# Performance work log

Measured on AMD Instinct MI355X. Metric: run time of the kernel, lower is better.

The kernel has to match this reference:

```python
import jax, jax.numpy as jnp
import numpy as np

DIM = 768
NUM_HEADS = 12
N_TOKENS = 4096


def setup_inputs() -> dict:
    key = jax.random.key(0)
    k_x, k_qkv, k_proj, k_pb = jax.random.split(key, 4)
    x = jax.random.normal(k_x, (N_TOKENS, DIM), dtype=jnp.float32)
    # nn.Linear(dim, dim*3, bias=False): weight shape (3*dim, dim)
    w_qkv = jax.random.normal(k_qkv, (3 * DIM, DIM), dtype=jnp.float32) * (DIM ** -0.5)
    # nn.Linear(dim, dim): weight (dim, dim), bias (dim,)
    w_proj = jax.random.normal(k_proj, (DIM, DIM), dtype=jnp.float32) * (DIM ** -0.5)
    b_proj = jax.random.normal(k_pb, (DIM,), dtype=jnp.float32) * 0.01
    return {"x": x, "w_qkv": w_qkv, "w_proj": w_proj, "b_proj": b_proj}


def reference(x, w_qkv, w_proj, b_proj):
    N, C = x.shape
    H = NUM_HEADS
    hd = C // H
    scale = hd ** -0.5
    qkv = (x @ w_qkv.T).reshape(N, 3, H, hd)  # (N, 3, H, hd)
    q = qkv[:, 0]  # (N, H, hd)
    k = qkv[:, 1]
    v = qkv[:, 2]
    # full NxN score matrix per head, as in the original (non-flash) code
    attn = jnp.einsum("nhd,mhd->hnm", q, k) * scale  # (H, N, N)
    attn = jax.nn.softmax(attn, axis=-1)
    out = jnp.einsum("hnm,mhd->nhd", attn, v).reshape(N, C)  # (N, C)
    return out @ w_proj.T + b_proj
```

## Files before the change

kernel.cpp:

```cpp
#include <hip/hip_runtime.h>
#include <hip/hip_bf16.h>

typedef __bf16 bf16_t;
typedef __attribute__((ext_vector_type(8))) __bf16 bf16x8;
typedef __attribute__((ext_vector_type(4))) __bf16 bf16x4;
typedef __attribute__((ext_vector_type(4))) short s16x4;
typedef __attribute__((ext_vector_type(4))) float f32x4;
typedef __attribute__((ext_vector_type(4))) _Float16 f16x4;

#define NTOK 4096
#define DIM  768
#define NH   12
#define HD   64
#define NSPLIT 4
#define KHALF (NTOK / NSPLIT)
#define XSZ  (NTOK * DIM)
#define WQSZ (3 * DIM * DIM)
#define WPSZ (DIM * DIM)
#define SCALE_L2E 0.18033688011112042f
#define SOFTMAX_C 12.0f

__device__ __forceinline__ bf16x8 load8(const bf16_t* p) {
    return *reinterpret_cast<const bf16x8*>(p);
}
__device__ __forceinline__ void store8(bf16_t* p, bf16x8 v) {
    *reinterpret_cast<bf16x8*>(p) = v;
}
__device__ __forceinline__ void gl2lds16(const bf16_t* g, bf16_t* l) {
    __builtin_amdgcn_global_load_lds(
        (const __attribute__((address_space(1))) void*)g,
        (__attribute__((address_space(3))) void*)l, 16, 0, 0);
}

__global__ __launch_bounds__(256) void cvt_kernel(
    const float* __restrict__ x, const float* __restrict__ wq,
    const float* __restrict__ wp,
    bf16_t* __restrict__ xb, bf16_t* __restrict__ wqb, bf16_t* __restrict__ wpb)
{
    size_t i = ((size_t)blockIdx.x * 256 + threadIdx.x) * 4;
    const float* src; bf16_t* dst; size_t off;
    if (i < XSZ)             { src = x;  dst = xb;  off = i; }
    else if (i < XSZ + WQSZ) { src = wq; dst = wqb; off = i - XSZ; }
    else                     { src = wp; dst = wpb; off = i - XSZ - WQSZ; }
    float4 v = *reinterpret_cast<const float4*>(src + off);
    bf16x4 o = { (bf16_t)v.x, (bf16_t)v.y, (bf16_t)v.z, (bf16_t)v.w };
    *reinterpret_cast<bf16x4*>(dst + off) = o;
}

__global__ __launch_bounds__(256) void qkv_gemm_kernel(
    const bf16_t* __restrict__ X, const bf16_t* __restrict__ W,
    bf16_t* __restrict__ Qo, bf16_t* __restrict__ Ko, bf16_t* __restrict__ Vt)
{
    __shared__ __align__(16) bf16_t As[128 * 32];
    __shared__ __align__(16) bf16_t Bs[128 * 32];
    const int tid  = threadIdx.x;
    const int wave = tid >> 6, lane = tid & 63;
    const int lr = lane & 15, lq = lane >> 4;
    const int M0 = blockIdx.x * 128;
    const int N0 = blockIdx.y * 128;
    const int wm = (wave >> 1) * 64, wn = (wave & 1) * 64;

    const int g_row = wave * 32 + (lane >> 2);
    const int g_col = (lane & 3) * 8;

    f32x4 acc[4][4] = {};

    for (int k0 = 0; k0 < DIM; k0 += 32) {
        #pragma unroll
        for (int c = 0; c < 2; ++c) {
            gl2lds16(&X[(size_t)(M0 + g_row + c * 16) * DIM + k0 + g_col],
                     &As[(wave * 32 + c * 16) * 32]);
            gl2lds16(&W[(size_t)(N0 + g_row + c * 16) * DIM + k0 + g_col],
                     &Bs[(wave * 32 + c * 16) * 32]);
        }
        __syncthreads();
        bf16x8 af[4], bfr[4];
        #pragma unroll
        for (int i = 0; i < 4; ++i) af[i]  = load8(&As[(wm + i * 16 + lr) * 32 + lq * 8]);
        #pragma unroll
        for (int i = 0; i < 4; ++i) bfr[i] = load8(&Bs[(wn + i * 16 + lr) * 32 + lq * 8]);
        #pragma unroll
        for (int r = 0; r < 4; ++r)
            #pragma unroll
            for (int c = 0; c < 4; ++c)
                acc[r][c] = __builtin_amdgcn_mfma_f32_16x16x32_bf16(af[r], bfr[c], acc[r][c], 0, 0, 0);
        __syncthreads();
    }

    const int t = N0 / DIM;
    if (t == 2) {
        #pragma unroll
        for (int r = 0; r < 4; ++r)
            #pragma unroll
            for (int c = 0; c < 4; ++c) {
                int m0 = M0 + wm + r * 16 + lq * 4;
                int rem = N0 + wn + c * 16 + lr - 2 * DIM;
                int hh = rem >> 6, d = rem & 63;
                bf16x4 v = { (bf16_t)acc[r][c][0], (bf16_t)acc[r][c][1],
                             (bf16_t)acc[r][c][2], (bf16_t)acc[r][c][3] };
                *reinterpret_cast<bf16x4*>(&Vt[((size_t)hh * HD + d) * NTOK + m0]) = v;
            }
    } else {
        #pragma unroll
        for (int r = 0; r < 4; ++r)
            #pragma unroll
            for (int c = 0; c < 4; ++c)
                #pragma unroll
                for (int reg = 0; reg < 4; ++reg) {
                    int m = M0 + wm + r * 16 + lq * 4 + reg;
                    int rem = N0 + wn + c * 16 + lr - t * DIM;
                    int hh = rem >> 6, d = rem & 63;
                    float v = acc[r][c][reg];
                    if (t == 0) Qo[(hh * NTOK + m) * HD + d] = (bf16_t)(v * SCALE_L2E);
                    else        Ko[(hh * NTOK + m) * HD + d] = (bf16_t)v;
                }
    }
}

__global__ __launch_bounds__(256) void flash_attn_kernel(
    const bf16_t* __restrict__ Qb, const bf16_t* __restrict__ Kb,
    const bf16_t* __restrict__ Vtb, _Float16* __restrict__ Opart,
    float* __restrict__ Lpart)
{
    __shared__ __align__(16) bf16_t Ks[2][64 * 64];
    __shared__ __align__(16) bf16_t Vs[2][64 * 64];
    const int tid  = threadIdx.x;
    const int wave = tid >> 6, lane = tid & 63;
    const int lr = lane & 15, lq = lane >> 4;
    const int h  = blockIdx.y;
    const int q0 = blockIdx.x * 128;
    const int sp = blockIdx.z;
    const int kt0 = sp * KHALF;
    const int NIT = KHALF / 64;

    const int sw_st = ((tid & 7) ^ ((tid >> 3) & 7)) * 8;
    const int kc0   = (lq ^ (lr & 7)) * 8;
    const int kc1   = ((4 + lq) ^ (lr & 7)) * 8;
    int vc[4];
    #pragma unroll
    for (int g = 0; g < 4; ++g)
        vc[g] = ((2 * g + (lq >> 1)) ^ (lr & 7)) * 8 + (lq & 1) * 4;

    const bf16_t* qrowA = &Qb[((size_t)h * NTOK + q0 + wave * 32 + lr) * HD];
    const bf16_t* qrowB = qrowA + 16 * HD;
    bf16x8 qa0 = load8(&qrowA[lq * 8]);
    bf16x8 qa1 = load8(&qrowA[32 + lq * 8]);
    bf16x8 qb0 = load8(&qrowB[lq * 8]);
    bf16x8 qb1 = load8(&qrowB[32 + lq * 8]);

    float la = 0.f, lb = 0.f;
    f32x4 oA[4] = {}, oB[4] = {};
    const f32x4 mc = { -SOFTMAX_C, -SOFTMAX_C, -SOFTMAX_C, -SOFTMAX_C };

    const int srA = tid >> 3;
    const int scA = (tid & 7) * 8;
    const bf16_t* kbase = &Kb[(size_t)h * NTOK * HD];
    const bf16_t* vbase = &Vtb[(size_t)h * HD * NTOK];

    bf16x8 pk0 = load8(&kbase[(size_t)(kt0 + srA) * HD + scA]);
    bf16x8 pk1 = load8(&kbase[(size_t)(kt0 + srA + 32) * HD + scA]);
    bf16x8 pv0 = load8(&vbase[(size_t)srA * NTOK + kt0 + scA]);
    bf16x8 pv1 = load8(&vbase[(size_t)(srA + 32) * NTOK + kt0 + scA]);

    for (int it = 0; it < NIT; ++it) {
        const int kt  = kt0 + it * 64;
        const int buf = it & 1;
        store8(&Ks[buf][srA * 64 + sw_st],        pk0);
        store8(&Ks[buf][(srA + 32) * 64 + sw_st], pk1);
        store8(&Vs[buf][srA * 64 + sw_st],        pv0);
        store8(&Vs[buf][(srA + 32) * 64 + sw_st], pv1);
        __syncthreads();

        if (it + 1 < NIT) {
            const int kn = kt + 64;
            pk0 = load8(&kbase[(size_t)(kn + srA) * HD + scA]);
            pk1 = load8(&kbase[(size_t)(kn + srA + 32) * HD + scA]);
            pv0 = load8(&vbase[(size_t)srA * NTOK + kn + scA]);
            pv1 = load8(&vbase[(size_t)(srA + 32) * NTOK + kn + scA]);
        }

        f32x4 sa[4], sb[4];
        __builtin_amdgcn_s_setprio(1);
        #pragma unroll
        for (int g = 0; g < 4; ++g) {
            bf16x8 k0 = load8(&Ks[buf][(g * 16 + lr) * 64 + kc0]);
            bf16x8 k1 = load8(&Ks[buf][(g * 16 + lr) * 64 + kc1]);
            f32x4 za = mc, zb = mc;
            za = __builtin_amdgcn_mfma_f32_16x16x32_bf16(k0, qa0, za, 0, 0, 0);
            za = __builtin_amdgcn_mfma_f32_16x16x32_bf16(k1, qa1, za, 0, 0, 0);
            zb = __builtin_amdgcn_mfma_f32_16x16x32_bf16(k0, qb0, zb, 0, 0, 0);
            zb = __builtin_amdgcn_mfma_f32_16x16x32_bf16(k1, qb1, zb, 0, 0, 0);
            sa[g] = za; sb[g] = zb;
        }
        __builtin_amdgcn_s_setprio(0);

        #pragma unroll
        for (int g = 0; g < 4; ++g)
            #pragma unroll
            for (int r = 0; r < 4; ++r) {
                sa[g][r] = __builtin_amdgcn_exp2f(sa[g][r]);
                la += sa[g][r];
                sb[g][r] = __builtin_amdgcn_exp2f(sb[g][r]);
                lb += sb[g][r];
            }

        __builtin_amdgcn_s_setprio(1);
        #pragma unroll
        for (int g = 0; g < 4; ++g) {
            bf16x4 pa = { (bf16_t)sa[g][0], (bf16_t)sa[g][1],
                          (bf16_t)sa[g][2], (bf16_t)sa[g][3] };
            bf16x4 pb = { (bf16_t)sb[g][0], (bf16_t)sb[g][1],
                          (bf16_t)sb[g][2], (bf16_t)sb[g][3] };
            s16x4 psa = __builtin_bit_cast(s16x4, pa);
            s16x4 psb = __builtin_bit_cast(s16x4, pb);
            #pragma unroll
            for (int dt = 0; dt < 4; ++dt) {
                s16x4 va = *reinterpret_cast<const s16x4*>(
                    &Vs[buf][(dt * 16 + lr) * 64 + vc[g]]);
                oA[dt] = __builtin_amdgcn_mfma_f32_16x16x16bf16_1k(va, psa, oA[dt], 0, 0, 0);
                oB[dt] = __builtin_amdgcn_mfma_f32_16x16x16bf16_1k(va, psb, oB[dt], 0, 0, 0);
            }
        }
        __builtin_amdgcn_s_setprio(0);
    }

    la += __shfl_xor(la, 16); la += __shfl_xor(la, 32);
    lb += __shfl_xor(lb, 16); lb += __shfl_xor(lb, 32);
    const int ma = q0 + wave * 32 + lr;
    const int mb = ma + 16;
    if (lq == 0) {
        Lpart[((size_t)sp * NH + h) * NTOK + ma] = la;
        Lpart[((size_t)sp * NH + h) * NTOK + mb] = lb;
    }
    _Float16* oa = &Opart[((size_t)sp * NTOK + ma) * DIM + h * HD];
    _Float16* ob = &Opart[((size_t)sp * NTOK + mb) * DIM + h * HD];
    #pragma unroll
    for (int dt = 0; dt < 4; ++dt) {
        f16x4 va = { (_Float16)oA[dt][0], (_Float16)oA[dt][1],
                     (_Float16)oA[dt][2], (_Float16)oA[dt][3] };
        f16x4 vb = { (_Float16)oB[dt][0], (_Float16)oB[dt][1],
                     (_Float16)oB[dt][2], (_Float16)oB[dt][3] };
        *reinterpret_cast<f16x4*>(&oa[dt * 16 + lq * 4]) = va;
        *reinterpret_cast<f16x4*>(&ob[dt * 16 + lq * 4]) = vb;
    }
}

__global__ __launch_bounds__(256) void combine_kernel(
    const _Float16* __restrict__ Opart, const float* __restrict__ Lpart,
    bf16_t* __restrict__ Ab)
{
    int idx = blockIdx.x * 256 + threadIdx.x;
    int m = idx / (DIM / 4);
    int c = (idx - m * (DIM / 4)) * 4;
    int hh = c >> 6;
    float l = 0.f;
    #pragma unroll
    for (int s = 0; s < NSPLIT; ++s)
        l += Lpart[((size_t)s * NH + hh) * NTOK + m];
    float rv = 1.f / l;
    float a0 = 0.f, a1 = 0.f, a2 = 0.f, a3 = 0.f;
    #pragma unroll
    for (int s = 0; s < NSPLIT; ++s) {
        f16x4 v = *reinterpret_cast<const f16x4*>(
            &Opart[((size_t)s * NTOK + m) * DIM + c]);
        a0 += (float)v[0]; a1 += (float)v[1];
        a2 += (float)v[2]; a3 += (float)v[3];
    }
    bf16x4 o = { (bf16_t)(a0 * rv), (bf16_t)(a1 * rv),
                 (bf16_t)(a2 * rv), (bf16_t)(a3 * rv) };
    *reinterpret_cast<bf16x4*>(&Ab[(size_t)m * DIM + c]) = o;
}

__global__ __launch_bounds__(256) void proj_gemm_kernel(
    const bf16_t* __restrict__ A, const bf16_t* __restrict__ W,
    const float* __restrict__ bias, float* __restrict__ out)
{
    __shared__ __align__(16) bf16_t As[64 * 32];
    __shared__ __align__(16) bf16_t Bs[64 * 32];
    const int tid  = threadIdx.x;
    const int wave = tid >> 6, lane = tid & 63;
    const int lr = lane & 15, lq = lane >> 4;
    const int M0 = blockIdx.x * 64;
    const int N0 = blockIdx.y * 64;
    const int wr = (wave >> 1) * 32, wc = (wave & 1) * 32;
    const int g_row = tid >> 2;
    const int g_col = (tid & 3) * 8;

    f32x4 acc[2][2] = {};

    for (int k0 = 0; k0 < DIM; k0 += 32) {
        gl2lds16(&A[(size_t)(M0 + g_row) * DIM + k0 + g_col], &As[wave * 512]);
        gl2lds16(&W[(size_t)(N0 + g_row) * DIM + k0 + g_col], &Bs[wave * 512]);
        __syncthreads();
        bf16x8 a0 = load8(&As[(wr + lr) * 32 + lq * 8]);
        bf16x8 a1 = load8(&As[(wr + 16 + lr) * 32 + lq * 8]);
        bf16x8 b0 = load8(&Bs[(wc + lr) * 32 + lq * 8]);
        bf16x8 b1 = load8(&Bs[(wc + 16 + lr) * 32 + lq * 8]);
        acc[0][0] = __builtin_amdgcn_mfma_f32_16x16x32_bf16(a0, b0, acc[0][0], 0, 0, 0);
        acc[0][1] = __builtin_amdgcn_mfma_f32_16x16x32_bf16(a0, b1, acc[0][1], 0, 0, 0);
        acc[1][0] = __builtin_amdgcn_mfma_f32_16x16x32_bf16(a1, b0, acc[1][0], 0, 0, 0);
        acc[1][1] = __builtin_amdgcn_mfma_f32_16x16x32_bf16(a1, b1, acc[1][1], 0, 0, 0);
        __syncthreads();
    }

    #pragma unroll
    for (int r = 0; r < 2; ++r)
        #pragma unroll
        for (int c = 0; c < 2; ++c)
            #pragma unroll
            for (int reg = 0; reg < 4; ++reg) {
                int m = M0 + wr + r * 16 + lq * 4 + reg;
                int n = N0 + wc + c * 16 + lr;
                out[(size_t)m * DIM + n] = acc[r][c][reg] + bias[n];
            }
}

extern "C" void kernel_launch(void* const* d_in, const int* in_sizes, int n_in,
                              void* d_out, int out_size, void* d_ws, size_t ws_size,
                              hipStream_t stream)
{
    const float* x      = (const float*)d_in[0];
    const float* w_qkv  = (const float*)d_in[1];
    const float* w_proj = (const float*)d_in[2];
    const float* b_proj = (const float*)d_in[3];
    float* out = (float*)d_out;

    char* ws = (char*)d_ws;
    const size_t sz = (size_t)NH * NTOK * HD * sizeof(bf16_t);
    bf16_t*   Q     = (bf16_t*)(ws);
    bf16_t*   K     = (bf16_t*)(ws + sz);
    bf16_t*   Vt    = (bf16_t*)(ws + 2 * sz);
    bf16_t*   xb    = (bf16_t*)(ws + 3 * sz);
    bf16_t*   wqb   = (bf16_t*)(ws + 3 * sz + (size_t)XSZ * 2);
    bf16_t*   wpb   = (bf16_t*)(ws + 3 * sz + (size_t)(XSZ + WQSZ) * 2);
    _Float16* Opart = (_Float16*)(ws + 3 * sz + (size_t)(XSZ + WQSZ + WPSZ) * 2);
    float*    Lpart = (float*)xb;
    bf16_t*   Ab    = Q;

    cvt_kernel<<<dim3((XSZ + WQSZ + WPSZ) / 1024), 256, 0, stream>>>(
        x, w_qkv, w_proj, xb, wqb, wpb);
    qkv_gemm_kernel<<<dim3(NTOK / 128, (3 * DIM) / 128), 256, 0, stream>>>(
        xb, wqb, Q, K, Vt);
    flash_attn_kernel<<<dim3(NTOK / 128, NH, NSPLIT), 256, 0, stream>>>(
        Q, K, Vt, Opart, Lpart);
    combine_kernel<<<dim3((NTOK * DIM / 4) / 256), 256, 0, stream>>>(
        Opart, Lpart, Ab);
    proj_gemm_kernel<<<dim3(NTOK / 64, DIM / 64), 256, 0, stream>>>(
        Ab, wpb, b_proj, out);
}
```

Baseline: 187.7 us.

## Use direct global-to-LDS loads and interleave QK, exp and PV per group

```diff
diff --git a/kernel.cpp b/kernel.cpp
--- a/kernel.cpp
+++ b/kernel.cpp
@@ -133,13 +133,23 @@
     const int kt0 = sp * KHALF;
     const int NIT = KHALF / 64;
 
-    const int sw_st = ((tid & 7) ^ ((tid >> 3) & 7)) * 8;
-    const int kc0   = (lq ^ (lr & 7)) * 8;
-    const int kc1   = ((4 + lq) ^ (lr & 7)) * 8;
+    const int kc0 = (lq ^ (lr & 7)) * 8;
+    const int kc1 = ((4 + lq) ^ (lr & 7)) * 8;
     int vc[4];
     #pragma unroll
     for (int g = 0; g < 4; ++g)
         vc[g] = ((2 * g + (lq >> 1)) ^ (lr & 7)) * 8 + (lq & 1) * 4;
+
+    const int srow = lane >> 3;
+    const int scol = ((lane & 7) ^ srow) * 8;
+    const bf16_t* kbase = &Kb[(size_t)h * NTOK * HD];
+    const bf16_t* vbase = &Vtb[(size_t)h * HD * NTOK];
+    const size_t kofA = (size_t)(wave * 16 + srow) * HD + scol;
+    const size_t kofB = kofA + (size_t)8 * HD;
+    const size_t vofA = (size_t)(wave * 16 + srow) * NTOK + scol;
+    const size_t vofB = vofA + (size_t)8 * NTOK;
+    const int ldA = (wave * 16) * 64;
+    const int ldB = (wave * 16 + 8) * 64;
 
     const bf16_t* qrowA = &Qb[((size_t)h * NTOK + q0 + wave * 32 + lr) * HD];
     const bf16_t* qrowB = qrowA + 16 * HD;
@@ -152,67 +162,54 @@
     f32x4 oA[4] = {}, oB[4] = {};
     const f32x4 mc = { -SOFTMAX_C, -SOFTMAX_C, -SOFTMAX_C, -SOFTMAX_C };
 
-    const int srA = tid >> 3;
-    const int scA = (tid & 7) * 8;
-    const bf16_t* kbase = &Kb[(size_t)h * NTOK * HD];
-    const bf16_t* vbase = &Vtb[(size_t)h * HD * NTOK];
-
-    bf16x8 pk0 = load8(&kbase[(size_t)(kt0 + srA) * HD + scA]);
-    bf16x8 pk1 = load8(&kbase[(size_t)(kt0 + srA + 32) * HD + scA]);
-    bf16x8 pv0 = load8(&vbase[(size_t)srA * NTOK + kt0 + scA]);
-    bf16x8 pv1 = load8(&vbase[(size_t)(srA + 32) * NTOK + kt0 + scA]);
+    {
+        const bf16_t* kp = kbase + (size_t)kt0 * HD;
+        const bf16_t* vp = vbase + kt0;
+        gl2lds16(kp + kofA, &Ks[0][ldA]);
+        gl2lds16(kp + kofB, &Ks[0][ldB]);
+        gl2lds16(vp + vofA, &Vs[0][ldA]);
+        gl2lds16(vp + vofB, &Vs[0][ldB]);
+    }
+    __syncthreads();
 
     for (int it = 0; it < NIT; ++it) {
-        const int kt  = kt0 + it * 64;
         const int buf = it & 1;
-        store8(&Ks[buf][srA * 64 + sw_st],        pk0);
-        store8(&Ks[buf][(srA + 32) * 64 + sw_st], pk1);
-        store8(&Vs[buf][srA * 64 + sw_st],        pv0);
-        store8(&Vs[buf][(srA + 32) * 64 + sw_st], pv1);
-        __syncthreads();
 
         if (it + 1 < NIT) {
-            const int kn = kt + 64;
-            pk0 = load8(&kbase[(size_t)(kn + srA) * HD + scA]);
-            pk1 = load8(&kbase[(size_t)(kn + srA + 32) * HD + scA]);
-            pv0 = load8(&vbase[(size_t)srA * NTOK + kn + scA]);
-            pv1 = load8(&vbase[(size_t)(srA + 32) * NTOK + kn + scA]);
+            const int kn = kt0 + (it + 1) * 64;
+            const bf16_t* kp = kbase + (size_t)kn * HD;
+            const bf16_t* vp = vbase + kn;
+            gl2lds16(kp + kofA, &Ks[buf ^ 1][ldA]);
+            gl2lds16(kp + kofB, &Ks[buf ^ 1][ldB]);
+            gl2lds16(vp + vofA, &Vs[buf ^ 1][ldA]);
+            gl2lds16(vp + vofB, &Vs[buf ^ 1][ldB]);
         }
 
-        f32x4 sa[4], sb[4];
-        __builtin_amdgcn_s_setprio(1);
         #pragma unroll
         for (int g = 0; g < 4; ++g) {
             bf16x8 k0 = load8(&Ks[buf][(g * 16 + lr) * 64 + kc0]);
             bf16x8 k1 = load8(&Ks[buf][(g * 16 + lr) * 64 + kc1]);
             f32x4 za = mc, zb = mc;
+            __builtin_amdgcn_s_setprio(1);
             za = __builtin_amdgcn_mfma_f32_16x16x32_bf16(k0, qa0, za, 0, 0, 0);
             za = __builtin_amdgcn_mfma_f32_16x16x32_bf16(k1, qa1, za, 0, 0, 0);
             zb = __builtin_amdgcn_mfma_f32_16x16x32_bf16(k0, qb0, zb, 0, 0, 0);
             zb = __builtin_amdgcn_mfma_f32_16x16x32_bf16(k1, qb1, zb, 0, 0, 0);
-            sa[g] = za; sb[g] = zb;
-        }
-        __builtin_amdgcn_s_setprio(0);
-
-        #pragma unroll
-        for (int g = 0; g < 4; ++g)
+            __builtin_amdgcn_s_setprio(0);
             #pragma unroll
             for (int r = 0; r < 4; ++r) {
-                sa[g][r] = __builtin_amdgcn_exp2f(sa[g][r]);
-                la += sa[g][r];
-                sb[g][r] = __builtin_amdgcn_exp2f(sb[g][r]);
-                lb += sb[g][r];
+                za[r] = __builtin_amdgcn_exp2f(za[r]);
+                la += za[r];
+                zb[r] = __builtin_amdgcn_exp2f(zb[r]);
+                lb += zb[r];
             }
-
-        __builtin_amdgcn_s_setprio(1);
-        #pragma unroll
-        for (int g = 0; g < 4; ++g) {
-            bf16x4 pa = { (bf16_t)sa[g][0], (bf16_t)sa[g][1],
-                          (bf16_t)sa[g][2], (bf16_t)sa[g][3] };
-            bf16x4 pb = { (bf16_t)sb[g][0], (bf16_t)sb[g][1],
-                          (bf16_t)sb[g][2], (bf16_t)sb[g][3] };
+            bf16x4 pa = { (bf16_t)za[0], (bf16_t)za[1],
+                          (bf16_t)za[2], (bf16_t)za[3] };
+            bf16x4 pb = { (bf16_t)zb[0], (bf16_t)zb[1],
+                          (bf16_t)zb[2], (bf16_t)zb[3] };
             s16x4 psa = __builtin_bit_cast(s16x4, pa);
             s16x4 psb = __builtin_bit_cast(s16x4, pb);
+            __builtin_amdgcn_s_setprio(1);
             #pragma unroll
             for (int dt = 0; dt < 4; ++dt) {
                 s16x4 va = *reinterpret_cast<const s16x4*>(
@@ -220,8 +217,10 @@
                 oA[dt] = __builtin_amdgcn_mfma_f32_16x16x16bf16_1k(va, psa, oA[dt], 0, 0, 0);
                 oB[dt] = __builtin_amdgcn_mfma_f32_16x16x16bf16_1k(va, psb, oB[dt], 0, 0, 0);
             }
+            __builtin_amdgcn_s_setprio(0);
         }
-        __builtin_amdgcn_s_setprio(0);
+
+        __syncthreads();
     }
 
     la += __shfl_xor(la, 16); la += __shfl_xor(la, 32);
```

Measured after the change: 187.7 us. No clear change (+0.0%).
